# Kernel tuning notes

Measured on AMD Instinct MI355X. Metric: run time of the kernel, lower is better.

## Reference

```python
import jax, jax.numpy as jnp
import numpy as np

B, FRAMES, NBINS, HOP = 4, 400, 129, 240
T = FRAMES * HOP  # 96000


def hann_window(K, dtype=jnp.float32):
    # torch.hann_window default is periodic=True: 0.5*(1 - cos(2*pi*n/K))
    n = jnp.arange(K, dtype=dtype)
    return 0.5 - 0.5 * jnp.cos(2.0 * jnp.pi * n / K)


def get_minimum_phase_fir(log_mag):
    # log_mag: [B, F, NBINS] -> full spectrum [B, F, N], N = 2*(NBINS-1)
    full = jnp.concatenate([log_mag, jnp.flip(log_mag, -1)[..., 1:-1]], axis=-1)
    N = full.shape[-1]
    # Hilbert transform (scipy-style analytic signal), N even
    Xf = jnp.fft.fft(full, axis=-1)
    h = jnp.concatenate([
        jnp.ones((1,), full.dtype),
        2.0 * jnp.ones((N // 2 - 1,), full.dtype),
        jnp.ones((1,), full.dtype),
        jnp.zeros((N // 2 - 1,), full.dtype),
    ])
    analytic = jnp.fft.ifft(Xf * h, axis=-1)
    min_phase = -jnp.imag(analytic)
    freq_resp = jnp.exp(full + 1j * min_phase)
    return jnp.real(jnp.fft.ifft(freq_resp, axis=-1))  # [B, F, N]


def windowing(kernel):
    K = kernel.shape[-1]
    w = hann_window(K, kernel.dtype)
    w = w.at[: K // 2].set(1.0)
    return kernel * w


def upsample_linear(x, scale):
    # x: [B, K, L] -> [B, K, L*scale], matches F.upsample(mode='linear', align_corners=False)
    L = x.shape[-1]
    out = jnp.arange(L * scale, dtype=x.dtype)
    src = jnp.clip((out + 0.5) / scale - 0.5, 0.0, L - 1.0)
    lo = jnp.floor(src).astype(jnp.int32)
    hi = jnp.minimum(lo + 1, L - 1)
    w = src - lo.astype(x.dtype)
    return x[..., lo] * (1.0 - w) + x[..., hi] * w


def fir_filt(x, h):
    # x: [B, T], h: [B, T, K]; causal time-varying FIR: y[t] = sum_k h[t,k] * x[t-k]
    K = h.shape[-1]
    Tn = x.shape[-1]
    x_pad = jnp.pad(x, ((0, 0), (K - 1, 0)))
    idx = jnp.arange(Tn)[:, None] + jnp.arange(K)[None, :]  # [T, K]
    frames = x_pad[:, idx]  # [B, T, K] (im2col-like gather)
    return jnp.einsum('btk,btk->bt', frames, jnp.flip(h, -1))


def setup_inputs() -> dict:
    key = jax.random.key(0)
    k1, k2 = jax.random.split(key)
    ex = jax.random.normal(k1, (B, T), dtype=jnp.float32)
    log_mag = jax.random.normal(k2, (B, FRAMES, NBINS), dtype=jnp.float32)
    return {"ex": ex, "log_mag": log_mag, "hop_length": HOP}


def reference(ex, log_mag, hop_length):
    kernel = get_minimum_phase_fir(log_mag)          # [B, F, K]
    kernel = windowing(kernel)
    up = upsample_linear(jnp.transpose(kernel, (0, 2, 1)), hop_length)  # [B, K, F*hop]
    up = jnp.transpose(up, (0, 2, 1))                # [B, F*hop, K]
    Tn = min(ex.shape[1], up.shape[1])
    ex = ex[:, :Tn]
    up = up[:, :Tn]
    return fir_filt(ex, up)
```

## Files before the change

kernel.cpp:

```cpp
#include <hip/hip_runtime.h>
#include <math.h>

#define NB 4
#define FRAMES 400
#define NBINS 129
#define HOP 240
#define T_LEN (FRAMES * HOP)
#define KLEN 256

#define REC_C { const float cn = fmaf(a2, cm, -cm1); cm1 = cm; cm = cn; }
#define REC_S { const float sn = fmaf(a2, sm, -sm1); sm1 = sm; sm = sn; }

__global__ __launch_bounds__(128) void gen_fir(const float* __restrict__ log_mag,
                                               float* __restrict__ kern) {
    const int bf = blockIdx.x;
    const int n  = threadIdx.x;

    __shared__ __align__(16) float  full[132];
    __shared__ __align__(16) float  g[128];
    __shared__ __align__(16) float2 crci[128];

    const float* lm = log_mag + bf * NBINS;
    full[n] = lm[n];
    if (n == 0) full[128] = lm[128];

    const float rev_n = (float)n * (1.0f / 256.0f);
    const float ca = __builtin_amdgcn_cosf(rev_n);
    const float sa = __builtin_amdgcn_sinf(rev_n);
    const float a2  = 2.0f * ca;
    const float sgn = (n & 1) ? -1.0f : 1.0f;
    __syncthreads();

    const float full0   = full[0];
    const float full128 = full[128];

    {
        const float4* f4p = (const float4*)full;
        float cm1 = ca, cm = 1.0f, acc = 0.0f;
#pragma unroll 8
        for (int u = 0; u < 32; ++u) {
            const float4 f4 = f4p[u];
            acc = fmaf(f4.x, cm, acc); REC_C;
            acc = fmaf(f4.y, cm, acc); REC_C;
            acc = fmaf(f4.z, cm, acc); REC_C;
            acc = fmaf(f4.w, cm, acc); REC_C;
        }
        const float Xf = 2.0f * acc - full0 + sgn * full128;
        g[n] = Xf * (1.0f / 128.0f);
    }
    __syncthreads();

    {
        const float4* g4p = (const float4*)g;
        float sm1 = -sa, sm = 0.0f, acc = 0.0f;
#pragma unroll 8
        for (int u = 0; u < 32; ++u) {
            const float4 gv = g4p[u];
            acc = fmaf(gv.x, sm, acc); REC_S;
            acc = fmaf(gv.y, sm, acc); REC_S;
            acc = fmaf(gv.z, sm, acc); REC_S;
            acc = fmaf(gv.w, sm, acc); REC_S;
        }
        const float mp = -acc;
        const float e  = __builtin_amdgcn_exp2f(full[n] * 1.4426950408889634f);
        float rev = mp * 0.15915494309189535f;
        rev = rev - floorf(rev);
        const float smp  = __builtin_amdgcn_sinf(rev);
        const float cmp_ = __builtin_amdgcn_cosf(rev);
        const float sc = (n == 0) ? 1.0f : 2.0f;
        crci[n] = make_float2(sc * e * cmp_, sc * e * smp);
    }
    __syncthreads();

    {
        const float e128 = __builtin_amdgcn_exp2f(full128 * 1.4426950408889634f);
        const float4* cc4 = (const float4*)crci;
        float cm1 = ca, cm = 1.0f;
        float sm1 = -sa, sm = 0.0f;
        float accE = 0.0f, accO = 0.0f;
#pragma unroll 8
        for (int u = 0; u < 64; ++u) {
            const float4 q = cc4[u];
            accE = fmaf(q.x, cm, accE); accE = fmaf(-q.y, sm, accE);
            REC_C; REC_S;
            accO = fmaf(q.z, cm, accO); accO = fmaf(-q.w, sm, accO);
            REC_C; REC_S;
        }
        const float base = sgn * e128;
        const float s = 1.0f / 256.0f;
        kern[bf * KLEN + n]       = (accE + accO + base) * s;
        kern[bf * KLEN + n + 128] = (accE - accO + base) * s * (0.5f + 0.5f * ca);
    }
}

__global__ __launch_bounds__(128) void fir_apply(const float* __restrict__ ex,
                                                 const float* __restrict__ kern,
                                                 float* __restrict__ out) {
    const int b   = blockIdx.y;
    const int bs  = blockIdx.x;
    const int tid = threadIdx.x;

    const int start = (bs == 0) ? 0 : 240 * bs - 120;
    const int end   = min(T_LEN, 240 * bs + 120);
    const int f     = (bs == 0) ? 0 : bs - 1;
    const int fh    = min(f + 1, FRAMES - 1);

    __shared__ float xs[496];

    const float* xb = ex + b * T_LEN;
    for (int i = tid; i < 496; i += 128) {
        const int t = start - 255 + i;
        xs[i] = (t >= 0 && t < T_LEN) ? xb[t] : 0.0f;
    }
    __syncthreads();

    const int te = start + 2 * tid;
    if (te >= end) return;

    float se = ((float)te + 0.5f) * (1.0f / HOP) - 0.5f;
    se = fminf(fmaxf(se, 0.0f), (float)(FRAMES - 1));
    float so = ((float)te + 1.5f) * (1.0f / HOP) - 0.5f;
    so = fminf(fmaxf(so, 0.0f), (float)(FRAMES - 1));
    const float we = se - (float)f;
    const float wo = so - (float)f;

    const float* kL = kern + (b * FRAMES + f)  * KLEN;
    const float* kH = kern + (b * FRAMES + fh) * KLEN;

    const int base = 2 * tid;
    float carry = xs[base + 256];
    float aeL = 0.0f, aeH = 0.0f, aoL = 0.0f, aoH = 0.0f;
#pragma unroll 4
    for (int u = 0; u < 64; ++u) {
        const float2 v1 = *(const float2*)&xs[base + 254 - 4 * u];
        const float2 v0 = *(const float2*)&xs[base + 252 - 4 * u];
        const float4 kl4 = *(const float4*)(kL + 4 * u);
        const float4 kh4 = *(const float4*)(kH + 4 * u);
        aeL = fmaf(v1.y,  kl4.x, aeL); aeH = fmaf(v1.y,  kh4.x, aeH);
        aoL = fmaf(carry, kl4.x, aoL); aoH = fmaf(carry, kh4.x, aoH);
        aeL = fmaf(v1.x,  kl4.y, aeL); aeH = fmaf(v1.x,  kh4.y, aeH);
        aoL = fmaf(v1.y,  kl4.y, aoL); aoH = fmaf(v1.y,  kh4.y, aoH);
        aeL = fmaf(v0.y,  kl4.z, aeL); aeH = fmaf(v0.y,  kh4.z, aeH);
        aoL = fmaf(v1.x,  kl4.z, aoL); aoH = fmaf(v1.x,  kh4.z, aoH);
        aeL = fmaf(v0.x,  kl4.w, aeL); aeH = fmaf(v0.x,  kh4.w, aeH);
        aoL = fmaf(v0.y,  kl4.w, aoL); aoH = fmaf(v0.y,  kh4.w, aoH);
        carry = v0.x;
    }

    const float y0 = aeL + we * (aeH - aeL);
    const float y1 = aoL + wo * (aoH - aoL);
    *(float2*)(out + b * T_LEN + te) = make_float2(y0, y1);
}

extern "C" void kernel_launch(void* const* d_in, const int* in_sizes, int n_in,
                              void* d_out, int out_size, void* d_ws, size_t ws_size,
                              hipStream_t stream) {
    const float* ex      = (const float*)d_in[0];
    const float* log_mag = (const float*)d_in[1];
    float* kern = (float*)d_ws;
    float* out  = (float*)d_out;

    gen_fir<<<NB * FRAMES, 128, 0, stream>>>(log_mag, kern);

    dim3 grid(401, NB);
    fir_apply<<<grid, 128, 0, stream>>>(ex, kern, out);
}
```

Before: 25.95 us.

## Halve gen_fir threads by computing paired DFT outputs per thread

gen_fir now runs 64 threads per frame instead of 128. Each thread computes two or four DFT outputs (n, n+64, n+128, n+192) from one cos/sin recurrence by using the symmetry of twiddle factors under quarter- and half-period shifts. The first stage reads log_mag straight from global memory instead of staging it in shared memory, which removes one barrier. This is meant to share recurrence work and cut wave count, at the cost of more registers and longer serial work per thread.

```diff
diff --git a/kernel.cpp b/kernel.cpp
--- a/kernel.cpp
+++ b/kernel.cpp
@@ -11,85 +11,93 @@
 #define REC_C { const float cn = fmaf(a2, cm, -cm1); cm1 = cm; cm = cn; }
 #define REC_S { const float sn = fmaf(a2, sm, -sm1); sm1 = sm; sm = sn; }
 
-__global__ __launch_bounds__(128) void gen_fir(const float* __restrict__ log_mag,
-                                               float* __restrict__ kern) {
+__global__ __launch_bounds__(64) void gen_fir(const float* __restrict__ log_mag,
+                                              float* __restrict__ kern) {
     const int bf = blockIdx.x;
     const int n  = threadIdx.x;
 
-    __shared__ __align__(16) float  full[132];
     __shared__ __align__(16) float  g[128];
     __shared__ __align__(16) float2 crci[128];
 
     const float* lm = log_mag + bf * NBINS;
-    full[n] = lm[n];
-    if (n == 0) full[128] = lm[128];
+
+    const float lmn0 = lm[n];
+    const float lmn1 = lm[n + 64];
 
     const float rev_n = (float)n * (1.0f / 256.0f);
     const float ca = __builtin_amdgcn_cosf(rev_n);
     const float sa = __builtin_amdgcn_sinf(rev_n);
     const float a2  = 2.0f * ca;
     const float sgn = (n & 1) ? -1.0f : 1.0f;
-    __syncthreads();
 
-    const float full0   = full[0];
-    const float full128 = full[128];
+    const float f0s  = lm[0];
+    const float f128 = lm[128];
 
     {
-        const float4* f4p = (const float4*)full;
-        float cm1 = ca, cm = 1.0f, acc = 0.0f;
-#pragma unroll 8
+        float cm1 = ca, cm = 1.0f, sm1 = -sa, sm = 0.0f;
+        float U = 0.0f, V = 0.0f;
+#pragma unroll
         for (int u = 0; u < 32; ++u) {
-            const float4 f4 = f4p[u];
-            acc = fmaf(f4.x, cm, acc); REC_C;
-            acc = fmaf(f4.y, cm, acc); REC_C;
-            acc = fmaf(f4.z, cm, acc); REC_C;
-            acc = fmaf(f4.w, cm, acc); REC_C;
+            float f;
+            f = lm[4 * u + 0]; U = fmaf(f, cm, U); V = fmaf(f, cm, V);  REC_C; REC_S;
+            f = lm[4 * u + 1]; U = fmaf(f, cm, U); V = fmaf(-f, sm, V); REC_C; REC_S;
+            f = lm[4 * u + 2]; U = fmaf(f, cm, U); V = fmaf(-f, cm, V); REC_C; REC_S;
+            f = lm[4 * u + 3]; U = fmaf(f, cm, U); V = fmaf(f, sm, V);  REC_C; REC_S;
         }
-        const float Xf = 2.0f * acc - full0 + sgn * full128;
-        g[n] = Xf * (1.0f / 128.0f);
+        const float base = -f0s + sgn * f128;
+        g[n]      = (base + 2.0f * U) * (1.0f / 128.0f);
+        g[n + 64] = (base + 2.0f * V) * (1.0f / 128.0f);
     }
     __syncthreads();
 
     {
         const float4* g4p = (const float4*)g;
-        float sm1 = -sa, sm = 0.0f, acc = 0.0f;
-#pragma unroll 8
+        float cm1 = ca, cm = 1.0f, sm1 = -sa, sm = 0.0f;
+        float U = 0.0f, V = 0.0f;
+#pragma unroll
         for (int u = 0; u < 32; ++u) {
             const float4 gv = g4p[u];
-            acc = fmaf(gv.x, sm, acc); REC_S;
-            acc = fmaf(gv.y, sm, acc); REC_S;
-            acc = fmaf(gv.z, sm, acc); REC_S;
-            acc = fmaf(gv.w, sm, acc); REC_S;
+            U = fmaf(gv.x, sm, U); V = fmaf(gv.x, sm, V);  REC_C; REC_S;
+            U = fmaf(gv.y, sm, U); V = fmaf(gv.y, cm, V);  REC_C; REC_S;
+            U = fmaf(gv.z, sm, U); V = fmaf(-gv.z, sm, V); REC_C; REC_S;
+            U = fmaf(gv.w, sm, U); V = fmaf(-gv.w, cm, V); REC_C; REC_S;
         }
-        const float mp = -acc;
-        const float e  = __builtin_amdgcn_exp2f(full[n] * 1.4426950408889634f);
-        float rev = mp * 0.15915494309189535f;
-        rev = rev - floorf(rev);
-        const float smp  = __builtin_amdgcn_sinf(rev);
-        const float cmp_ = __builtin_amdgcn_cosf(rev);
-        const float sc = (n == 0) ? 1.0f : 2.0f;
-        crci[n] = make_float2(sc * e * cmp_, sc * e * smp);
+        const float mp0 = -U, mp1 = -V;
+        const float e0 = __builtin_amdgcn_exp2f(lmn0 * 1.4426950408889634f);
+        const float e1 = __builtin_amdgcn_exp2f(lmn1 * 1.4426950408889634f);
+        float r0 = mp0 * 0.15915494309189535f; r0 -= floorf(r0);
+        float r1 = mp1 * 0.15915494309189535f; r1 -= floorf(r1);
+        const float w0 = (n == 0) ? 1.0f : 2.0f;
+        crci[n]      = make_float2(w0 * e0 * __builtin_amdgcn_cosf(r0),
+                                   w0 * e0 * __builtin_amdgcn_sinf(r0));
+        crci[n + 64] = make_float2(2.0f * e1 * __builtin_amdgcn_cosf(r1),
+                                   2.0f * e1 * __builtin_amdgcn_sinf(r1));
     }
     __syncthreads();
 
     {
-        const float e128 = __builtin_amdgcn_exp2f(full128 * 1.4426950408889634f);
         const float4* cc4 = (const float4*)crci;
-        float cm1 = ca, cm = 1.0f;
-        float sm1 = -sa, sm = 0.0f;
-        float accE = 0.0f, accO = 0.0f;
-#pragma unroll 8
-        for (int u = 0; u < 64; ++u) {
-            const float4 q = cc4[u];
-            accE = fmaf(q.x, cm, accE); accE = fmaf(-q.y, sm, accE);
-            REC_C; REC_S;
-            accO = fmaf(q.z, cm, accO); accO = fmaf(-q.w, sm, accO);
-            REC_C; REC_S;
+        float cm1 = ca, cm = 1.0f, sm1 = -sa, sm = 0.0f;
+        float W0 = 0.0f, W1 = 0.0f, W2 = 0.0f, W3 = 0.0f, X1 = 0.0f, X3 = 0.0f;
+#pragma unroll
+        for (int u = 0; u < 32; ++u) {
+            const float4 q1 = cc4[2 * u];
+            const float4 q2 = cc4[2 * u + 1];
+            W0 = fmaf(q1.x, cm, W0); W0 = fmaf(-q1.y, sm, W0); REC_C; REC_S;
+            W1 = fmaf(q1.z, cm, W1); W1 = fmaf(-q1.w, sm, W1);
+            X1 = fmaf(q1.z, sm, X1); X1 = fmaf(q1.w, cm, X1);  REC_C; REC_S;
+            W2 = fmaf(q2.x, cm, W2); W2 = fmaf(-q2.y, sm, W2); REC_C; REC_S;
+            W3 = fmaf(q2.z, cm, W3); W3 = fmaf(-q2.w, sm, W3);
+            X3 = fmaf(q2.z, sm, X3); X3 = fmaf(q2.w, cm, X3);  REC_C; REC_S;
         }
+        const float e128 = __builtin_amdgcn_exp2f(f128 * 1.4426950408889634f);
         const float base = sgn * e128;
         const float s = 1.0f / 256.0f;
-        kern[bf * KLEN + n]       = (accE + accO + base) * s;
-        kern[bf * KLEN + n + 128] = (accE - accO + base) * s * (0.5f + 0.5f * ca);
+        float* kp = kern + bf * KLEN;
+        kp[n]       = (W0 + W1 + W2 + W3 + base) * s;
+        kp[n + 64]  = (W0 - X1 - W2 + X3 + base) * s;
+        kp[n + 128] = (W0 - W1 + W2 - W3 + base) * s * (0.5f + 0.5f * ca);
+        kp[n + 192] = (W0 + X1 - W2 - X3 + base) * s * (0.5f - 0.5f * sa);
     }
 }
 
@@ -160,7 +168,7 @@
     float* kern = (float*)d_ws;
     float* out  = (float*)d_out;
 
-    gen_fir<<<NB * FRAMES, 128, 0, stream>>>(log_mag, kern);
+    gen_fir<<<NB * FRAMES, 64, 0, stream>>>(log_mag, kern);
 
     dim3 grid(401, NB);
     fir_apply<<<grid, 128, 0, stream>>>(ex, kern, out);
```

New measurement: 27.23 us. 1.05x slower.

## Broadcast DFT operands via readlane and software-prefetch FIR taps

Applied to the files above, without the earlier changes.

In the FIR generation kernel, the first DFT now reads log_mag directly from global memory, since every thread reads the same address and the load is uniform. The later DFT stages load one shared-memory value per lane and broadcast it with readlane, replacing the float4 shared-memory reads. In the FIR apply loop, the tap loads are double-buffered one iteration ahead and eight taps are handled per iteration. The aim is to cut LDS traffic and hide global load latency, at the cost of more scalar or readlane instructions and more registers.

```diff
diff --git a/kernel.cpp b/kernel.cpp
--- a/kernel.cpp
+++ b/kernel.cpp
@@ -8,84 +8,101 @@
 #define T_LEN (FRAMES * HOP)
 #define KLEN 256
 
-#define REC_C { const float cn = fmaf(a2, cm, -cm1); cm1 = cm; cm = cn; }
-#define REC_S { const float sn = fmaf(a2, sm, -sm1); sm1 = sm; sm = sn; }
+#define REC_C { const float cn_ = fmaf(a2, cm, -cm1); cm1 = cm; cm = cn_; }
+#define REC_S { const float sn_ = fmaf(a2, sm, -sm1); sm1 = sm; sm = sn_; }
+
+__device__ __forceinline__ float rlane(float v, int lane) {
+    return __uint_as_float(__builtin_amdgcn_readlane(__float_as_uint(v), lane));
+}
 
 __global__ __launch_bounds__(128) void gen_fir(const float* __restrict__ log_mag,
                                                float* __restrict__ kern) {
-    const int bf = blockIdx.x;
-    const int n  = threadIdx.x;
-
-    __shared__ __align__(16) float  full[132];
-    __shared__ __align__(16) float  g[128];
-    __shared__ __align__(16) float2 crci[128];
+    const int bf   = blockIdx.x;
+    const int n    = threadIdx.x;
+    const int lane = n & 63;
+
+    __shared__ float g[128];
+    __shared__ float crR[128];
+    __shared__ float ciR[128];
 
     const float* lm = log_mag + bf * NBINS;
-    full[n] = lm[n];
-    if (n == 0) full[128] = lm[128];
-
+
+    const float lmn = lm[n];
     const float rev_n = (float)n * (1.0f / 256.0f);
     const float ca = __builtin_amdgcn_cosf(rev_n);
     const float sa = __builtin_amdgcn_sinf(rev_n);
     const float a2  = 2.0f * ca;
     const float sgn = (n & 1) ? -1.0f : 1.0f;
-    __syncthreads();
-
-    const float full0   = full[0];
-    const float full128 = full[128];
+
+    const float full0   = lm[0];
+    const float full128 = lm[128];
 
     {
-        const float4* f4p = (const float4*)full;
         float cm1 = ca, cm = 1.0f, acc = 0.0f;
 #pragma unroll 8
-        for (int u = 0; u < 32; ++u) {
-            const float4 f4 = f4p[u];
-            acc = fmaf(f4.x, cm, acc); REC_C;
-            acc = fmaf(f4.y, cm, acc); REC_C;
-            acc = fmaf(f4.z, cm, acc); REC_C;
-            acc = fmaf(f4.w, cm, acc); REC_C;
-        }
-        const float Xf = 2.0f * acc - full0 + sgn * full128;
-        g[n] = Xf * (1.0f / 128.0f);
+        for (int m = 0; m < 128; ++m) {
+            acc = fmaf(lm[m], cm, acc);
+            REC_C;
+        }
+        g[n] = (2.0f * acc - full0 + sgn * full128) * (1.0f / 128.0f);
     }
     __syncthreads();
 
     {
-        const float4* g4p = (const float4*)g;
+        const float gq0 = g[lane], gq1 = g[lane + 64];
         float sm1 = -sa, sm = 0.0f, acc = 0.0f;
-#pragma unroll 8
-        for (int u = 0; u < 32; ++u) {
-            const float4 gv = g4p[u];
-            acc = fmaf(gv.x, sm, acc); REC_S;
-            acc = fmaf(gv.y, sm, acc); REC_S;
-            acc = fmaf(gv.z, sm, acc); REC_S;
-            acc = fmaf(gv.w, sm, acc); REC_S;
+        for (int c = 0; c < 8; ++c) {
+#pragma unroll
+            for (int r = 0; r < 8; ++r) {
+                acc = fmaf(rlane(gq0, 8 * c + r), sm, acc); REC_S;
+            }
+        }
+        for (int c = 0; c < 8; ++c) {
+#pragma unroll
+            for (int r = 0; r < 8; ++r) {
+                acc = fmaf(rlane(gq1, 8 * c + r), sm, acc); REC_S;
+            }
         }
         const float mp = -acc;
-        const float e  = __builtin_amdgcn_exp2f(full[n] * 1.4426950408889634f);
+        const float e  = __builtin_amdgcn_exp2f(lmn * 1.4426950408889634f);
         float rev = mp * 0.15915494309189535f;
-        rev = rev - floorf(rev);
-        const float smp  = __builtin_amdgcn_sinf(rev);
-        const float cmp_ = __builtin_amdgcn_cosf(rev);
+        rev -= floorf(rev);
         const float sc = (n == 0) ? 1.0f : 2.0f;
-        crci[n] = make_float2(sc * e * cmp_, sc * e * smp);
+        crR[n] = sc * e * __builtin_amdgcn_cosf(rev);
+        ciR[n] = sc * e * __builtin_amdgcn_sinf(rev);
     }
     __syncthreads();
 
     {
+        const float cq0 = crR[lane], cq1 = crR[lane + 64];
+        const float sq0 = ciR[lane], sq1 = ciR[lane + 64];
+        float cm1 = ca, cm = 1.0f, sm1 = -sa, sm = 0.0f;
+        float accE = 0.0f, accO = 0.0f;
+        for (int c = 0; c < 8; ++c) {
+#pragma unroll
+            for (int r = 0; r < 8; r += 2) {
+                const int k = 8 * c + r;
+                accE = fmaf(rlane(cq0, k), cm, accE);
+                accE = fmaf(-rlane(sq0, k), sm, accE);
+                REC_C; REC_S;
+                accO = fmaf(rlane(cq0, k + 1), cm, accO);
+                accO = fmaf(-rlane(sq0, k + 1), sm, accO);
+                REC_C; REC_S;
+            }
+        }
+        for (int c = 0; c < 8; ++c) {
+#pragma unroll
+            for (int r = 0; r < 8; r += 2) {
+                const int k = 8 * c + r;
+                accE = fmaf(rlane(cq1, k), cm, accE);
+                accE = fmaf(-rlane(sq1, k), sm, accE);
+                REC_C; REC_S;
+                accO = fmaf(rlane(cq1, k + 1), cm, accO);
+                accO = fmaf(-rlane(sq1, k + 1), sm, accO);
+                REC_C; REC_S;
+            }
+        }
         const float e128 = __builtin_amdgcn_exp2f(full128 * 1.4426950408889634f);
-        const float4* cc4 = (const float4*)crci;
-        float cm1 = ca, cm = 1.0f;
-        float sm1 = -sa, sm = 0.0f;
-        float accE = 0.0f, accO = 0.0f;
-#pragma unroll 8
-        for (int u = 0; u < 64; ++u) {
-            const float4 q = cc4[u];
-            accE = fmaf(q.x, cm, accE); accE = fmaf(-q.y, sm, accE);
-            REC_C; REC_S;
-            accO = fmaf(q.z, cm, accO); accO = fmaf(-q.w, sm, accO);
-            REC_C; REC_S;
-        }
         const float base = sgn * e128;
         const float s = 1.0f / 256.0f;
         kern[bf * KLEN + n]       = (accE + accO + base) * s;
@@ -124,26 +141,45 @@
     const float we = se - (float)f;
     const float wo = so - (float)f;
 
-    const float* kL = kern + (b * FRAMES + f)  * KLEN;
-    const float* kH = kern + (b * FRAMES + fh) * KLEN;
+    const float4* kL4 = (const float4*)(kern + (b * FRAMES + f)  * KLEN);
+    const float4* kH4 = (const float4*)(kern + (b * FRAMES + fh) * KLEN);
 
     const int base = 2 * tid;
     float carry = xs[base + 256];
     float aeL = 0.0f, aeH = 0.0f, aoL = 0.0f, aoH = 0.0f;
+
+    float4 plA = kL4[0], plB = kL4[1], phA = kH4[0], phB = kH4[1];
+
 #pragma unroll 4
-    for (int u = 0; u < 64; ++u) {
-        const float2 v1 = *(const float2*)&xs[base + 254 - 4 * u];
-        const float2 v0 = *(const float2*)&xs[base + 252 - 4 * u];
-        const float4 kl4 = *(const float4*)(kL + 4 * u);
-        const float4 kh4 = *(const float4*)(kH + 4 * u);
-        aeL = fmaf(v1.y,  kl4.x, aeL); aeH = fmaf(v1.y,  kh4.x, aeH);
-        aoL = fmaf(carry, kl4.x, aoL); aoH = fmaf(carry, kh4.x, aoH);
-        aeL = fmaf(v1.x,  kl4.y, aeL); aeH = fmaf(v1.x,  kh4.y, aeH);
-        aoL = fmaf(v1.y,  kl4.y, aoL); aoH = fmaf(v1.y,  kh4.y, aoH);
-        aeL = fmaf(v0.y,  kl4.z, aeL); aeH = fmaf(v0.y,  kh4.z, aeH);
-        aoL = fmaf(v1.x,  kl4.z, aoL); aoH = fmaf(v1.x,  kh4.z, aoH);
-        aeL = fmaf(v0.x,  kl4.w, aeL); aeH = fmaf(v0.x,  kh4.w, aeH);
-        aoL = fmaf(v0.y,  kl4.w, aoL); aoH = fmaf(v0.y,  kh4.w, aoH);
+    for (int c = 0; c < 32; ++c) {
+        const float4 klA = plA, klB = plB, khA = phA, khB = phB;
+        const int cn = (c + 1) & 31;
+        plA = kL4[2 * cn]; plB = kL4[2 * cn + 1];
+        phA = kH4[2 * cn]; phB = kH4[2 * cn + 1];
+
+        const int p = base + 248 - 8 * c;
+        const float2 v0 = *(const float2*)&xs[p];
+        const float2 v1 = *(const float2*)&xs[p + 2];
+        const float2 v2 = *(const float2*)&xs[p + 4];
+        const float2 v3 = *(const float2*)&xs[p + 6];
+
+        aeL = fmaf(v3.y,  klA.x, aeL); aeH = fmaf(v3.y,  khA.x, aeH);
+        aoL = fmaf(carry, klA.x, aoL); aoH = fmaf(carry, khA.x, aoH);
+        aeL = fmaf(v3.x,  klA.y, aeL); aeH = fmaf(v3.x,  khA.y, aeH);
+        aoL = fmaf(v3.y,  klA.y, aoL); aoH = fmaf(v3.y,  khA.y, aoH);
+        aeL = fmaf(v2.y,  klA.z, aeL); aeH = fmaf(v2.y,  khA.z, aeH);
+        aoL = fmaf(v3.x,  klA.z, aoL); aoH = fmaf(v3.x,  khA.z, aoH);
+        aeL = fmaf(v2.x,  klA.w, aeL); aeH = fmaf(v2.x,  khA.w, aeH);
+        aoL = fmaf(v2.y,  klA.w, aoL); aoH = fmaf(v2.y,  khA.w, aoH);
+        aeL = fmaf(v1.y,  klB.x, aeL); aeH = fmaf(v1.y,  khB.x, aeH);
+        aoL = fmaf(v2.x,  klB.x, aoL); aoH = fmaf(v2.x,  khB.x, aoH);
+        aeL = fmaf(v1.x,  klB.y, aeL); aeH = fmaf(v1.x,  khB.y, aeH);
+        aoL = fmaf(v1.y,  klB.y, aoL); aoH = fmaf(v1.y,  khB.y, aoH);
+        aeL = fmaf(v0.y,  klB.z, aeL); aeH = fmaf(v0.y,  khB.z, aeH);
+        aoL = fmaf(v1.x,  klB.z, aoL); aoH = fmaf(v1.x,  khB.z, aoH);
+        aeL = fmaf(v0.x,  klB.w, aeL); aeH = fmaf(v0.x,  khB.w, aeH);
+        aoL = fmaf(v0.y,  klB.w, aoL); aoH = fmaf(v0.y,  khB.w, aoH);
+
         carry = v0.x;
     }
 
```

After: 30.66 us. 1.18x slower.
